# Performance work log

Hardware: AMD Instinct MI355X
Metric: run time of the kernel (lower is better)

## Reference

```python
import jax, jax.numpy as jnp
import numpy as np

HID = 256   # hidden_dim
P = 16      # pool_size
EPS = 1e-5


def _ln(x, g, b):
    m = x.mean(-1, keepdims=True)
    v = x.var(-1, keepdims=True)
    return (x - m) * jax.lax.rsqrt(v + EPS) * g + b


def setup_inputs() -> dict:
    key = jax.random.key(0)
    ks = jax.random.split(key, 12)
    B, Cf, H, W = 8, 512, 64, 64
    Cg = Cf // 2
    Co = Cf // 2
    s = 0.02
    d = {}
    d['e_f'] = jax.random.normal(ks[0], (B, Cf, H, W), jnp.float32)
    d['e_g'] = jax.random.normal(ks[1], (B, Cg, H, W), jnp.float32)
    d['l_feat'] = jax.random.normal(ks[2], (B, 768, 20), jnp.float32)
    d['l_mask'] = jnp.ones((B, 20, 1), jnp.float32)
    d['ln_f_g'] = jnp.ones((Cf,), jnp.float32)
    d['ln_f_b'] = jnp.zeros((Cf,), jnp.float32)
    d['ln_g_g'] = jnp.ones((Cg,), jnp.float32)
    d['ln_g_b'] = jnp.zeros((Cg,), jnp.float32)
    d['wq'] = jax.random.normal(ks[3], (Cf, HID), jnp.float32) * s
    d['bq'] = jnp.zeros((HID,), jnp.float32)
    d['wk'] = jax.random.normal(ks[4], (Cg, HID), jnp.float32) * s
    d['bk'] = jnp.zeros((HID,), jnp.float32)
    d['wv'] = jax.random.normal(ks[5], (Cg, HID), jnp.float32) * s
    d['bv'] = jnp.zeros((HID,), jnp.float32)
    d['wo'] = jax.random.normal(ks[6], (HID, HID), jnp.float32) * s
    d['bo'] = jnp.zeros((HID,), jnp.float32)
    d['dw_k'] = jax.random.normal(ks[7], (HID, 1, 3, 3), jnp.float32) * s  # depthwise kernel (OIHW, I=1)
    d['efp_w'] = jax.random.normal(ks[8], (HID, Cf), jnp.float32) * s     # 1x1 conv v_channels->hidden
    d['efp_b'] = jnp.zeros((HID,), jnp.float32)
    d['outc_w'] = jax.random.normal(ks[9], (Co, HID), jnp.float32) * s    # 1x1 conv hidden->out
    d['outc_b'] = jnp.zeros((Co,), jnp.float32)
    d['bn_g'] = jnp.ones((Co,), jnp.float32)
    d['bn_b'] = jnp.zeros((Co,), jnp.float32)
    d['bn_m'] = jnp.zeros((Co,), jnp.float32)
    d['bn_v'] = jnp.ones((Co,), jnp.float32)
    return d


def reference(e_f, e_g, l_feat, l_mask, ln_f_g, ln_f_b, ln_g_g, ln_g_b,
              wq, bq, wk, bk, wv, bv, wo, bo, dw_k, efp_w, efp_b,
              outc_w, outc_b, bn_g, bn_b, bn_m, bn_v):
    B, Cf, H, W = e_f.shape
    # Q = w_qi(LN(e_f))                                  (B, HW, HID)
    q = _ln(e_f.transpose(0, 2, 3, 1), ln_f_g, ln_f_b).reshape(B, H * W, Cf) @ wq + bq
    # K/V projections from LN(e_g)
    g = _ln(e_g.transpose(0, 2, 3, 1), ln_g_g, ln_g_b).reshape(B, H * W, -1)
    k = (g @ wk + bk).reshape(B, H, W, HID)
    v = (g @ wv + bv).reshape(B, H, W, HID)
    # 16x16 max/avg pooling -> (B, Hp*Wp, HID)
    k = jnp.max(k.reshape(B, H // P, P, W // P, P, HID), axis=(2, 4)).reshape(B, -1, HID)
    v = jnp.mean(v.reshape(B, H // P, P, W // P, P, HID), axis=(2, 4)).reshape(B, -1, HID)
    # pooled attention
    attn = jax.nn.softmax(jnp.einsum('bqd,bkd->bqk', q, k) * (HID ** -0.5), axis=-1)
    a_i = jnp.einsum('bqk,bkd->bqd', attn, v)  # (B, HW, HID)
    # depthwise 3x3 conv on Q (NCHW)
    q_nchw = q.reshape(B, H, W, HID).transpose(0, 3, 1, 2)
    dw = jax.lax.conv_general_dilated(q_nchw, dw_k, (1, 1), [(1, 1), (1, 1)],
                                      feature_group_count=HID)
    combined = dw + a_i.reshape(B, H, W, HID).transpose(0, 3, 1, 2)
    comb = combined.transpose(0, 2, 3, 1).reshape(B, H * W, HID) @ wo + bo
    comb = comb.reshape(B, H, W, HID).transpose(0, 3, 1, 2)
    # 1x1 proj of e_f, elementwise gate
    efp = jnp.einsum('bchw,oc->bohw', e_f, efp_w) + efp_b[None, :, None, None]
    e_a = efp * comb
    # out: 1x1 conv + BN (inference) + ReLU (dropout inactive in eval)
    out = jnp.einsum('bchw,oc->bohw', e_a, outc_w) + outc_b[None, :, None, None]
    scale = (bn_g * jax.lax.rsqrt(bn_v + EPS))[None, :, None, None]
    out = (out - bn_m[None, :, None, None]) * scale + bn_b[None, :, None, None]
    return jax.nn.relu(out)
```

## Files before the change

### kernel.cpp

```cpp
#include <hip/hip_runtime.h>
#include <math.h>

#define EPS 1e-5f

typedef __attribute__((ext_vector_type(8))) short bf16x8;
typedef __attribute__((ext_vector_type(4))) float f32x4;

__device__ __forceinline__ unsigned short f2bf(float f) {
    unsigned int u = __float_as_uint(f);
    u += 0x7fff + ((u >> 16) & 1);
    return (unsigned short)(u >> 16);
}
__device__ __forceinline__ float bf2f(unsigned short h) {
    return __uint_as_float(((unsigned int)h) << 16);
}
__device__ __forceinline__ float lof(unsigned int u) {
    return __uint_as_float(u << 16);
}
__device__ __forceinline__ float hif(unsigned int u) {
    return __uint_as_float(u & 0xffff0000u);
}
__device__ __forceinline__ void async16(void* lds, const void* g) {
    __builtin_amdgcn_global_load_lds(
        (const __attribute__((address_space(1))) unsigned int*)g,
        (__attribute__((address_space(3))) unsigned int*)lds, 16, 0, 0);
}

__global__ __launch_bounds__(256) void prep_all(
    const float* __restrict__ lnfg, const float* __restrict__ lnfb,
    const float* __restrict__ wq, const float* __restrict__ bq,
    const float* __restrict__ efpw, const float* __restrict__ efpb,
    const float* __restrict__ lngg, const float* __restrict__ lngb,
    const float* __restrict__ wk, const float* __restrict__ bk,
    const float* __restrict__ wv, const float* __restrict__ bv,
    const float* __restrict__ wo, const float* __restrict__ outcw,
    const float* __restrict__ outcb, const float* __restrict__ bng,
    const float* __restrict__ bnb, const float* __restrict__ bnm,
    const float* __restrict__ bnv, const float* __restrict__ dwk,
    unsigned short* __restrict__ Wb1t, unsigned short* __restrict__ Wb2t,
    unsigned short* __restrict__ Wot, unsigned short* __restrict__ Woc,
    float* __restrict__ dwt,
    float* __restrict__ cs1, float* __restrict__ cst1,
    float* __restrict__ cs2, float* __restrict__ cst2,
    float* __restrict__ scv, float* __restrict__ shv)
{
    int idx = blockIdx.x * 256 + threadIdx.x;
    if (idx < 262144) {
        int n = idx >> 9, k = idx & 511;
        float v = (n < 256) ? lnfg[k] * wq[k * 256 + n]
                            : efpw[(size_t)(n - 256) * 512 + k];
        Wb1t[idx] = f2bf(v);
    } else if (idx < 327680) {
        int j = idx - 262144; int n = j >> 8, k = j & 255;
        Wb2t[j] = f2bf(lngg[k] * wk[k * 256 + n]);
    } else if (idx < 393216) {
        int j = idx - 327680; int n = j >> 8, k = j & 255;
        Wot[j] = f2bf(wo[k * 256 + n]);
    } else if (idx < 458752) {
        int j = idx - 393216;
        Woc[j] = f2bf(outcw[j]);
    } else if (idx < 461056) {
        int j = idx - 458752; int tap = j >> 8, ch = j & 255;
        dwt[j] = dwk[ch * 9 + tap];
    } else if (idx < 462336) {
        int j = idx - 461056;
        if (j < 256) {
            int n = j; float cs = 0.f, ct = 0.f;
            for (int k = 0; k < 512; k++) {
                float w = wq[k * 256 + n];
                cs += lnfg[k] * w; ct += lnfb[k] * w;
            }
            cs1[n] = cs; cst1[n] = ct + bq[n];
        } else if (j < 512) {
            cs1[j] = 0.f; cst1[j] = efpb[j - 256];
        } else if (j < 768) {
            int n = j - 512; float cs = 0.f, ct = 0.f;
            for (int k = 0; k < 256; k++) {
                float w = wk[k * 256 + n];
                cs += lngg[k] * w; ct += lngb[k] * w;
            }
            cs2[n] = cs; cst2[n] = ct + bk[n];
        } else if (j < 1024) {
            int n = j - 768; float cs = 0.f, ct = 0.f;
            for (int k = 0; k < 256; k++) {
                float w = wv[k * 256 + n];
                cs += lngg[k] * w; ct += lngb[k] * w;
            }
            cs2[256 + n] = cs; cst2[256 + n] = ct + bv[n];
        } else {
            int n = j - 1024;
            float s = bng[n] * rsqrtf(bnv[n] + EPS);
            scv[n] = s;
            shv[n] = (outcb[n] - bnm[n]) * s + bnb[n];
        }
    }
}

__global__ __launch_bounds__(256) void transpose_fg(
    const float* __restrict__ ef, const float* __restrict__ eg,
    unsigned short* __restrict__ ef_bf, unsigned short* __restrict__ eg_bf,
    float* __restrict__ pf, float* __restrict__ pfq,
    float* __restrict__ pg, float* __restrict__ pgq)
{
    __shared__ float tile[64][65];
    __shared__ float psum[4][64], pss[4][64];
    int id = blockIdx.x;
    const float* src; unsigned short* dst; float* ps; float* pq;
    int C, cblk, b, p0;
    if (id < 4096) {
        src = ef; dst = ef_bf; ps = pf; pq = pfq; C = 512;
        p0 = (id & 63) * 64; cblk = (id >> 6) & 7; b = id >> 9;
    } else {
        id -= 4096;
        src = eg; dst = eg_bf; ps = pg; pq = pgq; C = 256;
        p0 = (id & 63) * 64; cblk = (id >> 6) & 3; b = id >> 8;
    }
    int c0 = cblk * 64;
    const float* s = src + ((size_t)b * C + c0) * 4096 + p0;
    int t = threadIdx.x;

    int cr = t >> 4, p4 = (t & 15) * 4;
#pragma unroll
    for (int i = 0; i < 4; i++) {
        int c = i * 16 + cr;
        float4 v = *(const float4*)(s + (size_t)c * 4096 + p4);
        tile[c][p4 + 0] = v.x; tile[c][p4 + 1] = v.y;
        tile[c][p4 + 2] = v.z; tile[c][p4 + 3] = v.w;
    }
    __syncthreads();

    unsigned short* d = dst + ((size_t)(b * 4096 + p0)) * C + c0;
    int pr = t >> 3, c8 = (t & 7) * 8;
#pragma unroll
    for (int i = 0; i < 2; i++) {
        int p = i * 32 + pr;
        uint4 pk;
        pk.x = (unsigned)f2bf(tile[c8 + 0][p]) | ((unsigned)f2bf(tile[c8 + 1][p]) << 16);
        pk.y = (unsigned)f2bf(tile[c8 + 2][p]) | ((unsigned)f2bf(tile[c8 + 3][p]) << 16);
        pk.z = (unsigned)f2bf(tile[c8 + 4][p]) | ((unsigned)f2bf(tile[c8 + 5][p]) << 16);
        pk.w = (unsigned)f2bf(tile[c8 + 6][p]) | ((unsigned)f2bf(tile[c8 + 7][p]) << 16);
        *(uint4*)(d + (size_t)p * C + c8) = pk;
    }

    int lane = t & 63, grp = t >> 6;
    float sm = 0.f, sq = 0.f;
#pragma unroll
    for (int j = 0; j < 16; j++) {
        float v = tile[grp * 16 + j][lane];
        sm += v; sq += v * v;
    }
    psum[grp][lane] = sm; pss[grp][lane] = sq;
    __syncthreads();
    if (t < 64) {
        float fs = psum[0][t] + psum[1][t] + psum[2][t] + psum[3][t];
        float fq = pss[0][t] + pss[1][t] + pss[2][t] + pss[3][t];
        ps[cblk * 32768 + b * 4096 + p0 + t] = fs;
        pq[cblk * 32768 + b * 4096 + p0 + t] = fq;
    }
}

__global__ __launch_bounds__(256) void ln_finalize(
    const float* __restrict__ pf, const float* __restrict__ pfq,
    const float* __restrict__ pg, const float* __restrict__ pgq,
    float* __restrict__ mf, float* __restrict__ rf,
    float* __restrict__ mg, float* __restrict__ rg)
{
    int gp = blockIdx.x * 256 + threadIdx.x;
    float s = 0.f, q = 0.f;
#pragma unroll
    for (int i = 0; i < 8; i++) { s += pf[i * 32768 + gp]; q += pfq[i * 32768 + gp]; }
    float m = s * (1.f / 512.f);
    float v = q * (1.f / 512.f) - m * m;
    mf[gp] = m; rf[gp] = rsqrtf(v + EPS);
    s = 0.f; q = 0.f;
#pragma unroll
    for (int i = 0; i < 4; i++) { s += pg[i * 32768 + gp]; q += pgq[i * 32768 + gp]; }
    m = s * (1.f / 256.f);
    v = q * (1.f / 256.f) - m * m;
    mg[gp] = m; rg[gp] = rsqrtf(v + EPS);
}

template<int K>
__device__ __forceinline__ void mfma_core(
    const unsigned short* __restrict__ A, const unsigned short* __restrict__ Bt,
    int m0, int n0, unsigned short* As, unsigned short* Bs, f32x4 acc[4][4])
{
    const int tid = threadIdx.x;
    const int wave = tid >> 6, lane = tid & 63;
    const int wm = (wave & 1) * 64, wn = (wave >> 1) * 64;
#pragma unroll
    for (int i = 0; i < 4; i++)
#pragma unroll
        for (int j = 0; j < 4; j++) acc[i][j] = (f32x4){0.f, 0.f, 0.f, 0.f};

    const int srow = wave * 32 + (lane >> 3);
    const int sg = (lane & 7) ^ ((lane >> 3) & 7);
    const unsigned short* ga = A + (size_t)(m0 + srow) * K + sg * 8;
    const unsigned short* gb = Bt + (size_t)(n0 + srow) * K + sg * 8;

    for (int k0 = 0; k0 < K; k0 += 64) {
#pragma unroll
        for (int t = 0; t < 4; t++) {
            async16(As + (wave * 32 + t * 8) * 64, ga + (size_t)t * 8 * K + k0);
            async16(Bs + (wave * 32 + t * 8) * 64, gb + (size_t)t * 8 * K + k0);
        }
        __syncthreads();
#pragma unroll
        for (int ks = 0; ks < 2; ks++) {
            bf16x8 af[4], bfr[4];
            int kb = ks * 4 + (lane >> 4);
            int slot = (kb ^ (lane & 7)) * 8;
#pragma unroll
            for (int i = 0; i < 4; i++) {
                int m = wm + i * 16 + (lane & 15);
                af[i] = *(const bf16x8*)&As[m * 64 + slot];
                int n = wn + i * 16 + (lane & 15);
                bfr[i] = *(const bf16x8*)&Bs[n * 64 + slot];
            }
#pragma unroll
            for (int i = 0; i < 4; i++)
#pragma unroll
                for (int j = 0; j < 4; j++)
                    acc[i][j] = __builtin_amdgcn_mfma_f32_16x16x32_bf16(
                        af[i], bfr[j], acc[i][j], 0, 0, 0);
        }
        __syncthreads();
    }
}

__global__ __launch_bounds__(256) void gemm1_mfma(
    const unsigned short* __restrict__ ef_bf, const unsigned short* __restrict__ Wb1t,
    const float* __restrict__ cs1, const float* __restrict__ cst1,
    const float* __restrict__ mf, const float* __restrict__ rf,
    unsigned short* __restrict__ qbuf, unsigned short* __restrict__ efpbuf)
{
    __shared__ unsigned short As[8192], Bs[8192];
    f32x4 acc[4][4];
    int m0 = blockIdx.x * 128, n0 = blockIdx.y * 128;
    mfma_core<512>(ef_bf, Wb1t, m0, n0, As, Bs, acc);
    int lane = threadIdx.x & 63, wave = threadIdx.x >> 6;
    int wm = (wave & 1) * 64, wn = (wave >> 1) * 64;
    bool isq = (n0 < 256);
#pragma unroll
    for (int i = 0; i < 4; i++) {
#pragma unroll
        for (int r = 0; r < 4; r++) {
            int gm = m0 + wm + i * 16 + ((lane >> 4) * 4) + r;
            float mean = mf[gm], rs = rf[gm];
#pragma unroll
            for (int j = 0; j < 4; j++) {
                int n = n0 + wn + j * 16 + (lane & 15);
                float v = acc[i][j][r];
                if (isq) {
                    float o = rs * (v - mean * cs1[n]) + cst1[n];
                    qbuf[(size_t)gm * 256 + n] = f2bf(o);
                } else {
                    efpbuf[(size_t)gm * 256 + (n - 256)] = f2bf(v + cst1[n]);
                }
            }
        }
    }
}

__global__ __launch_bounds__(256) void gemm2k_mfma(
    const unsigned short* __restrict__ eg_bf, const unsigned short* __restrict__ Wb2t,
    const float* __restrict__ cs2, const float* __restrict__ cst2,
    const float* __restrict__ mg, const float* __restrict__ rg,
    unsigned short* __restrict__ kfull)
{
    __shared__ unsigned short As[8192], Bs[8192];
    f32x4 acc[4][4];
    int m0 = blockIdx.x * 128, n0 = blockIdx.y * 128;
    mfma_core<256>(eg_bf, Wb2t, m0, n0, As, Bs, acc);
    int lane = threadIdx.x & 63, wave = threadIdx.x >> 6;
    int wm = (wave & 1) * 64, wn = (wave >> 1) * 64;
#pragma unroll
    for (int i = 0; i < 4; i++) {
#pragma unroll
        for (int r = 0; r < 4; r++) {
            int gm = m0 + wm + i * 16 + ((lane >> 4) * 4) + r;
            float mean = mg[gm], rs = rg[gm];
#pragma unroll
            for (int j = 0; j < 4; j++) {
                int n = n0 + wn + j * 16 + (lane & 15);
                float o = rs * (acc[i][j][r] - mean * cs2[n]) + cst2[n];
                kfull[(size_t)gm * 256 + n] = f2bf(o);
            }
        }
    }
}

__global__ __launch_bounds__(256) void gemm34_mfma(
    const unsigned short* __restrict__ comb, const unsigned short* __restrict__ Wot,
    const float* __restrict__ bo, const unsigned short* __restrict__ efp,
    const unsigned short* __restrict__ Woc,
    const float* __restrict__ scv, const float* __restrict__ shv,
    float* __restrict__ outp)
{
    __shared__ unsigned short As[64 * 64];
    __shared__ unsigned short Bs[256 * 64];
    __shared__ unsigned short eat[64 * 256];
    const int tid = threadIdx.x;
    const int wave = tid >> 6, lane = tid & 63;
    const int m0 = blockIdx.x * 64;

    const int srow = lane >> 3;
    const int sg = (lane & 7) ^ (srow & 7);

    f32x4 acc[4][4];
#pragma unroll
    for (int i = 0; i < 4; i++)
#pragma unroll
        for (int j = 0; j < 4; j++) acc[i][j] = (f32x4){0.f, 0.f, 0.f, 0.f};

    const unsigned short* ga = comb + (size_t)(m0 + wave * 16 + srow) * 256 + sg * 8;
    const unsigned short* gb = Wot + (size_t)(wave * 64 + srow) * 256 + sg * 8;

    for (int k0 = 0; k0 < 256; k0 += 64) {
#pragma unroll
        for (int t = 0; t < 2; t++)
            async16(As + (wave * 16 + t * 8) * 64, ga + (size_t)t * 8 * 256 + k0);
#pragma unroll
        for (int t = 0; t < 8; t++)
            async16(Bs + (wave * 64 + t * 8) * 64, gb + (size_t)t * 8 * 256 + k0);
        __syncthreads();
#pragma unroll
        for (int ks = 0; ks < 2; ks++) {
            bf16x8 af[4], bfr[4];
            int kb = ks * 4 + (lane >> 4);
            int slot = (kb ^ (lane & 7)) * 8;
#pragma unroll
            for (int i = 0; i < 4; i++) {
                af[i]  = *(const bf16x8*)&As[(i * 16 + (lane & 15)) * 64 + slot];
                bfr[i] = *(const bf16x8*)&Bs[(wave * 64 + i * 16 + (lane & 15)) * 64 + slot];
            }
#pragma unroll
            for (int i = 0; i < 4; i++)
#pragma unroll
                for (int j = 0; j < 4; j++)
                    acc[i][j] = __builtin_amdgcn_mfma_f32_16x16x32_bf16(
                        af[i], bfr[j], acc[i][j], 0, 0, 0);
        }
        __syncthreads();
    }

    float bo4[4];
#pragma unroll
    for (int j = 0; j < 4; j++) bo4[j] = bo[wave * 64 + j * 16 + (lane & 15)];
#pragma unroll
    for (int i = 0; i < 4; i++) {
#pragma unroll
        for (int r = 0; r < 4; r++) {
            int pos = i * 16 + ((lane >> 4) * 4) + r;
#pragma unroll
            for (int j = 0; j < 4; j++) {
                int n = wave * 64 + j * 16 + (lane & 15);
                float o = (acc[i][j][r] + bo4[j])
                          * bf2f(efp[(size_t)(m0 + pos) * 256 + n]);
                int o8 = j * 2 + ((lane >> 3) & 1);
                int slot = o8 ^ (pos & 7);
                eat[pos * 256 + wave * 64 + slot * 8 + (lane & 7)] = f2bf(o);
            }
        }
    }

    f32x4 acc2[4][4];
#pragma unroll
    for (int i = 0; i < 4; i++)
#pragma unroll
        for (int j = 0; j < 4; j++) acc2[i][j] = (f32x4){0.f, 0.f, 0.f, 0.f};

    const unsigned short* gw = Woc + (size_t)(wave * 64 + srow) * 256 + sg * 8;
    for (int k0 = 0; k0 < 256; k0 += 64) {
#pragma unroll
        for (int t = 0; t < 8; t++)
            async16(Bs + (wave * 64 + t * 8) * 64, gw + (size_t)t * 8 * 256 + k0);
        __syncthreads();
        int kc = k0 >> 6;
#pragma unroll
        for (int ks = 0; ks < 2; ks++) {
            bf16x8 af2[4], bf2_[4];
            int kb = ks * 4 + (lane >> 4);
            int slot = (kb ^ (lane & 7)) * 8;
#pragma unroll
            for (int i = 0; i < 4; i++) {
                af2[i]  = *(const bf16x8*)&Bs[(wave * 64 + i * 16 + (lane & 15)) * 64 + slot];
                bf2_[i] = *(const bf16x8*)&eat[(i * 16 + (lane & 15)) * 256 + kc * 64 + slot];
            }
#pragma unroll
            for (int i = 0; i < 4; i++)
#pragma unroll
                for (int j = 0; j < 4; j++)
                    acc2[i][j] = __builtin_amdgcn_mfma_f32_16x16x32_bf16(
                        af2[i], bf2_[j], acc2[i][j], 0, 0, 0);
        }
        __syncthreads();
    }

#pragma unroll
    for (int i = 0; i < 4; i++) {
#pragma unroll
        for (int r = 0; r < 4; r++) {
            int co = wave * 64 + i * 16 + ((lane >> 4) * 4) + r;
            float s = scv[co], hh = shv[co];
#pragma unroll
            for (int j = 0; j < 4; j++) {
                int p = m0 + j * 16 + (lane & 15);
                float o = fmaxf(fmaf(acc2[i][j][r], s, hh), 0.f);
                outp[((size_t)(p >> 12)) * 1048576 + (size_t)co * 4096 + (p & 4095)] = o;
            }
        }
    }
}

__global__ __launch_bounds__(256) void pool_phase(
    const unsigned short* __restrict__ kfull, const float* __restrict__ eg,
    const float* __restrict__ rg, const float* __restrict__ mg,
    unsigned short* __restrict__ kpb, float* __restrict__ s1,
    float* __restrict__ s0)
{
    __shared__ float smem[4352];
    int id = blockIdx.x;
    int t = threadIdx.x;
    if (id < 128) {
        int b = id >> 4, cell = id & 15;
        int hp = cell >> 2, wp = cell & 3;
        int g8 = t & 31, rr = t >> 5;
        float kmx[8];
#pragma unroll
        for (int j = 0; j < 8; j++) kmx[j] = -3.402823466e38f;
#pragma unroll
        for (int rsub = 0; rsub < 2; rsub++) {
            int r = rr * 2 + rsub;
            int prow = (hp * 16 + r) * 64 + wp * 16;
            for (int cl = 0; cl < 16; cl++) {
                size_t basei = ((size_t)(b * 4096 + prow + cl)) * 256 + g8 * 8;
                uint4 kv = *(const uint4*)(kfull + basei);
                kmx[0] = fmaxf(kmx[0], lof(kv.x)); kmx[1] = fmaxf(kmx[1], hif(kv.x));
                kmx[2] = fmaxf(kmx[2], lof(kv.y)); kmx[3] = fmaxf(kmx[3], hif(kv.y));
                kmx[4] = fmaxf(kmx[4], lof(kv.z)); kmx[5] = fmaxf(kmx[5], hif(kv.z));
                kmx[6] = fmaxf(kmx[6], lof(kv.w)); kmx[7] = fmaxf(kmx[7], hif(kv.w));
            }
        }
#pragma unroll
        for (int j = 0; j < 8; j++) smem[rr * 256 + g8 * 8 + j] = kmx[j];
        __syncthreads();
        float m = smem[t];
#pragma unroll
        for (int r2 = 1; r2 < 8; r2++) m = fmaxf(m, smem[r2 * 256 + t]);
        kpb[(size_t)(b * 16 + cell) * 256 + t] = f2bf(m);
    } else {
        int id2 = id - 128;
        int b = id2 >> 6, hp = (id2 >> 4) & 3, cgrp = id2 & 15;
        int rr = t >> 4, cq = t & 15, cx = cq >> 2;
        int p = (hp * 16 + rr) * 64 + cq * 4;
        float4 w4 = *(const float4*)&rg[b * 4096 + p];
        float part[16];
        const float* egb = eg + ((size_t)b * 256 + cgrp * 16) * 4096 + p;
#pragma unroll
        for (int cc = 0; cc < 16; cc++) {
            float4 v4 = *(const float4*)(egb + (size_t)cc * 4096);
            part[cc] = w4.x * v4.x + w4.y * v4.y + w4.z * v4.z + w4.w * v4.w;
        }
#pragma unroll
        for (int cc = 0; cc < 16; cc++) smem[t * 16 + cc] = part[cc];
        if (cgrp == 0) {
            float4 m4 = *(const float4*)&mg[b * 4096 + p];
            smem[4096 + t] = w4.x * m4.x + w4.y * m4.y + w4.z * m4.z + w4.w * m4.w;
        }
        __syncthreads();
        if (t < 64) {
            int cx2 = t >> 4, cc = t & 15;
            float sacc = 0.f;
#pragma unroll
            for (int rr2 = 0; rr2 < 16; rr2++)
#pragma unroll
                for (int dq = 0; dq < 4; dq++)
                    sacc += smem[(rr2 * 16 + cx2 * 4 + dq) * 16 + cc];
            s1[((size_t)(b * 16 + hp * 4 + cx2)) * 256 + cgrp * 16 + cc] = sacc;
        }
        if (cgrp == 0 && t < 4) {
            float sacc = 0.f;
#pragma unroll
            for (int rr2 = 0; rr2 < 16; rr2++)
#pragma unroll
                for (int dq = 0; dq < 4; dq++)
                    sacc += smem[4096 + rr2 * 16 + t * 4 + dq];
            s0[b * 16 + hp * 4 + t] = sacc;
        }
    }
}

__global__ __launch_bounds__(256) void vpool_gemm(
    const float* __restrict__ s1, const float* __restrict__ s0,
    const float* __restrict__ lngg, const float* __restrict__ wv,
    const float* __restrict__ cs2, const float* __restrict__ cst2,
    float* __restrict__ vp)
{
    int cell = blockIdx.x;
    int n = threadIdx.x;
    const float* s1r = s1 + (size_t)cell * 256;
    float acc = 0.f;
    for (int c = 0; c < 256; c++)
        acc = fmaf(lngg[c] * s1r[c], wv[c * 256 + n], acc);
    vp[(size_t)cell * 256 + n] = acc * (1.f / 256.f)
        - (s0[cell] * (1.f / 256.f)) * cs2[256 + n] + cst2[256 + n];
}

__global__ __launch_bounds__(256) void combined_dw(
    const unsigned short* __restrict__ qbuf, const unsigned short* __restrict__ kpb,
    const float* __restrict__ vp, const float* __restrict__ dwt,
    unsigned short* __restrict__ combined)
{
    __shared__ float attns[256];
    int wave = threadIdx.x >> 6, lane = threadIdx.x & 63;
    int id = blockIdx.x;
    int b = id & 7, seg = id >> 3;
    int pidx0 = seg * 16;

    if (wave == 0) {
        int fr = lane & 15, quad = lane >> 4;
        const unsigned short* qrow = qbuf + (size_t)(b * 4096 + pidx0 + fr) * 256 + quad * 8;
        const unsigned short* krow = kpb + (size_t)(b * 16 + fr) * 256 + quad * 8;
        f32x4 sacc = {0.f, 0.f, 0.f, 0.f};
#pragma unroll
        for (int ks = 0; ks < 8; ks++) {
            bf16x8 af = *(const bf16x8*)(qrow + ks * 32);
            bf16x8 bf_ = *(const bf16x8*)(krow + ks * 32);
            sacc = __builtin_amdgcn_mfma_f32_16x16x32_bf16(af, bf_, sacc, 0, 0, 0);
        }
#pragma unroll
        for (int r = 0; r < 4; r++) {
            float s = sacc[r] * 0.0625f;
            float mx = s;
#pragma unroll
            for (int off = 8; off >= 1; off >>= 1) mx = fmaxf(mx, __shfl_xor(mx, off));
            float e = __expf(s - mx);
            float sum = e;
#pragma unroll
            for (int off = 8; off >= 1; off >>= 1) sum += __shfl_xor(sum, off);
            attns[(quad * 4 + r) * 16 + fr] = e / sum;
        }
    }
    __syncthreads();

    int pidx = pidx0 + wave * 4;
    int h = pidx >> 6, w0 = pidx & 63;
    int o4 = lane * 4;

    float4 kreg[9];
#pragma unroll
    for (int tap = 0; tap < 9; tap++)
        kreg[tap] = *(const float4*)&dwt[tap * 256 + o4];

    float4 acc[4];
#pragma unroll
    for (int i = 0; i < 4; i++) acc[i] = (float4){0.f, 0.f, 0.f, 0.f};

    const float* arow = attns + (wave * 4) * 16;
#pragma unroll
    for (int c = 0; c < 16; c++) {
        float4 v = *(const float4*)&vp[(size_t)(b * 16 + c) * 256 + o4];
#pragma unroll
        for (int i = 0; i < 4; i++) {
            float a = arow[i * 16 + c];
            acc[i].x = fmaf(a, v.x, acc[i].x); acc[i].y = fmaf(a, v.y, acc[i].y);
            acc[i].z = fmaf(a, v.z, acc[i].z); acc[i].w = fmaf(a, v.w, acc[i].w);
        }
    }
#pragma unroll
    for (int dy = 0; dy < 3; dy++) {
        int hh = h + dy - 1;
        if (hh < 0 || hh > 63) continue;
        const unsigned short* qr = qbuf + ((size_t)(b * 4096 + hh * 64)) * 256;
        float4 ft[6];
#pragma unroll
        for (int c = 0; c < 6; c++) {
            int xx = w0 - 1 + c;
            if (xx < 0 || xx > 63) {
                ft[c] = (float4){0.f, 0.f, 0.f, 0.f};
            } else {
                uint2 qa = *(const uint2*)(qr + (size_t)xx * 256 + o4);
                ft[c] = (float4){lof(qa.x), hif(qa.x), lof(qa.y), hif(qa.y)};
            }
        }
#pragma unroll
        for (int dx = 0; dx < 3; dx++) {
            float4 kk = kreg[dy * 3 + dx];
#pragma unroll
            for (int i = 0; i < 4; i++) {
                float4 qv = ft[i + dx];
                acc[i].x = fmaf(qv.x, kk.x, acc[i].x);
                acc[i].y = fmaf(qv.y, kk.y, acc[i].y);
                acc[i].z = fmaf(qv.z, kk.z, acc[i].z);
                acc[i].w = fmaf(qv.w, kk.w, acc[i].w);
            }
        }
    }
#pragma unroll
    for (int i = 0; i < 4; i++) {
        uint2 pk;
        pk.x = (unsigned)f2bf(acc[i].x) | ((unsigned)f2bf(acc[i].y) << 16);
        pk.y = (unsigned)f2bf(acc[i].z) | ((unsigned)f2bf(acc[i].w) << 16);
        *(uint2*)(combined + ((size_t)(b * 4096 + pidx + i)) * 256 + o4) = pk;
    }
}

extern "C" void kernel_launch(void* const* d_in, const int* in_sizes, int n_in,
                              void* d_out, int out_size, void* d_ws, size_t ws_size,
                              hipStream_t stream)
{
    const float* e_f   = (const float*)d_in[0];
    const float* e_g   = (const float*)d_in[1];
    const float* lnfg  = (const float*)d_in[4];
    const float* lnfb  = (const float*)d_in[5];
    const float* lngg  = (const float*)d_in[6];
    const float* lngb  = (const float*)d_in[7];
    const float* wq    = (const float*)d_in[8];
    const float* bq    = (const float*)d_in[9];
    const float* wk    = (const float*)d_in[10];
    const float* bk    = (const float*)d_in[11];
    const float* wv    = (const float*)d_in[12];
    const float* bv    = (const float*)d_in[13];
    const float* wo    = (const float*)d_in[14];
    const float* bo    = (const float*)d_in[15];
    const float* dwk   = (const float*)d_in[16];
    const float* efpw  = (const float*)d_in[17];
    const float* efpb  = (const float*)d_in[18];
    const float* outcw = (const float*)d_in[19];
    const float* outcb = (const float*)d_in[20];
    const float* bng   = (const float*)d_in[21];
    const float* bnb   = (const float*)d_in[22];
    const float* bnm   = (const float*)d_in[23];
    const float* bnv   = (const float*)d_in[24];
    float* outp = (float*)d_out;

    char* base = (char*)d_ws;
    auto alloc = [&](size_t bytes) -> char* {
        char* r = base; base += (bytes + 255) & ~(size_t)255; return r;
    };
    float* pf    = (float*)alloc(8 * 32768 * 4);
    float* pfq   = (float*)alloc(8 * 32768 * 4);
    float* pg    = (float*)alloc(4 * 32768 * 4);
    float* pgq   = (float*)alloc(4 * 32768 * 4);
    float* mf    = (float*)alloc(32768 * 4);
    float* rf    = (float*)alloc(32768 * 4);
    float* mg    = (float*)alloc(32768 * 4);
    float* rg    = (float*)alloc(32768 * 4);
    float* cs1   = (float*)alloc(512 * 4);
    float* cst1  = (float*)alloc(512 * 4);
    float* cs2   = (float*)alloc(512 * 4);
    float* cst2  = (float*)alloc(512 * 4);
    float* scv   = (float*)alloc(256 * 4);
    float* shv   = (float*)alloc(256 * 4);
    float* dwt   = (float*)alloc(9 * 256 * 4);
    unsigned short* Wb1t = (unsigned short*)alloc(262144 * 2);
    unsigned short* Wb2t = (unsigned short*)alloc(65536 * 2);
    unsigned short* Wot  = (unsigned short*)alloc(65536 * 2);
    unsigned short* Woc  = (unsigned short*)alloc(65536 * 2);
    unsigned short* ef_bf = (unsigned short*)alloc((size_t)32768 * 512 * 2);
    unsigned short* eg_bf = (unsigned short*)alloc((size_t)32768 * 256 * 2);
    unsigned short* qbuf  = (unsigned short*)alloc((size_t)32768 * 256 * 2);
    unsigned short* efpbuf = (unsigned short*)alloc((size_t)32768 * 256 * 2);
    unsigned short* kfull = (unsigned short*)alloc((size_t)32768 * 256 * 2);
    unsigned short* kpb  = (unsigned short*)alloc(128 * 256 * 2);
    float* vp    = (float*)alloc(128 * 256 * 4);
    float* s1    = (float*)alloc(128 * 256 * 4);
    float* s0    = (float*)alloc(128 * 4);

    prep_all<<<1806, 256, 0, stream>>>(
        lnfg, lnfb, wq, bq, efpw, efpb, lngg, lngb, wk, bk, wv, bv, wo,
        outcw, outcb, bng, bnb, bnm, bnv, dwk,
        Wb1t, Wb2t, Wot, Woc, dwt, cs1, cst1, cs2, cst2, scv, shv);
    transpose_fg<<<6144, 256, 0, stream>>>(e_f, e_g, ef_bf, eg_bf,
                                           pf, pfq, pg, pgq);
    ln_finalize<<<128, 256, 0, stream>>>(pf, pfq, pg, pgq, mf, rf, mg, rg);
    gemm1_mfma<<<dim3(256, 4), 256, 0, stream>>>(ef_bf, Wb1t, cs1, cst1, mf, rf,
                                                 qbuf, efpbuf);
    gemm2k_mfma<<<dim3(256, 2), 256, 0, stream>>>(eg_bf, Wb2t, cs2, cst2, mg, rg,
                                                  kfull);
    pool_phase<<<640, 256, 0, stream>>>(kfull, e_g, rg, mg, kpb, s1, s0);
    vpool_gemm<<<128, 256, 0, stream>>>(s1, s0, lngg, wv, cs2, cst2, vp);
    combined_dw<<<2048, 256, 0, stream>>>(qbuf, kpb, vp, dwt, kfull);
    gemm34_mfma<<<512, 256, 0, stream>>>(kfull, Wot, bo, efpbuf,
                                         Woc, scv, shv, outp);
}
```

Before: 323.5 us.

## Widen gemm1 tile to 128x256 and double transpose work per block

gemm1 now computes a 128x256 output tile per block, each wave holding 4x8 MFMA accumulators. This halves the number of passes over the A operand (ef_bf), and each block's tile lies entirely in either the Q or the efp half. The transpose kernel now has each block handle two 64-pixel tiles, issuing all global loads up front to hide latency and halving the block count. The trade-off is higher register and LDS use per block in gemm1, which may reduce occupancy, and an extra barrier in the transpose kernel.

```diff
diff --git a/kernel.cpp b/kernel.cpp
--- a/kernel.cpp
+++ b/kernel.cpp
@@ -107,55 +107,68 @@
     int id = blockIdx.x;
     const float* src; unsigned short* dst; float* ps; float* pq;
     int C, cblk, b, p0;
-    if (id < 4096) {
+    if (id < 2048) {
         src = ef; dst = ef_bf; ps = pf; pq = pfq; C = 512;
-        p0 = (id & 63) * 64; cblk = (id >> 6) & 7; b = id >> 9;
+        b = id >> 8; cblk = (id >> 5) & 7; p0 = (id & 31) * 128;
     } else {
-        id -= 4096;
+        id -= 2048;
         src = eg; dst = eg_bf; ps = pg; pq = pgq; C = 256;
-        p0 = (id & 63) * 64; cblk = (id >> 6) & 3; b = id >> 8;
+        b = id >> 7; cblk = (id >> 5) & 3; p0 = (id & 31) * 128;
     }
     int c0 = cblk * 64;
     const float* s = src + ((size_t)b * C + c0) * 4096 + p0;
     int t = threadIdx.x;
-
     int cr = t >> 4, p4 = (t & 15) * 4;
-#pragma unroll
-    for (int i = 0; i < 4; i++) {
-        int c = i * 16 + cr;
-        float4 v = *(const float4*)(s + (size_t)c * 4096 + p4);
-        tile[c][p4 + 0] = v.x; tile[c][p4 + 1] = v.y;
-        tile[c][p4 + 2] = v.z; tile[c][p4 + 3] = v.w;
-    }
-    __syncthreads();
-
-    unsigned short* d = dst + ((size_t)(b * 4096 + p0)) * C + c0;
+    int lane = t & 63, grp = t >> 6;
     int pr = t >> 3, c8 = (t & 7) * 8;
-#pragma unroll
-    for (int i = 0; i < 2; i++) {
-        int p = i * 32 + pr;
-        uint4 pk;
-        pk.x = (unsigned)f2bf(tile[c8 + 0][p]) | ((unsigned)f2bf(tile[c8 + 1][p]) << 16);
-        pk.y = (unsigned)f2bf(tile[c8 + 2][p]) | ((unsigned)f2bf(tile[c8 + 3][p]) << 16);
-        pk.z = (unsigned)f2bf(tile[c8 + 4][p]) | ((unsigned)f2bf(tile[c8 + 5][p]) << 16);
-        pk.w = (unsigned)f2bf(tile[c8 + 6][p]) | ((unsigned)f2bf(tile[c8 + 7][p]) << 16);
-        *(uint4*)(d + (size_t)p * C + c8) = pk;
-    }
-
-    int lane = t & 63, grp = t >> 6;
-    float sm = 0.f, sq = 0.f;
-#pragma unroll
-    for (int j = 0; j < 16; j++) {
-        float v = tile[grp * 16 + j][lane];
-        sm += v; sq += v * v;
-    }
-    psum[grp][lane] = sm; pss[grp][lane] = sq;
-    __syncthreads();
-    if (t < 64) {
-        float fs = psum[0][t] + psum[1][t] + psum[2][t] + psum[3][t];
-        float fq = pss[0][t] + pss[1][t] + pss[2][t] + pss[3][t];
-        ps[cblk * 32768 + b * 4096 + p0 + t] = fs;
-        pq[cblk * 32768 + b * 4096 + p0 + t] = fq;
+
+    float4 r1[4], r2[4];
+#pragma unroll
+    for (int i = 0; i < 4; i++)
+        r1[i] = *(const float4*)(s + (size_t)(i * 16 + cr) * 4096 + p4);
+#pragma unroll
+    for (int i = 0; i < 4; i++)
+        r2[i] = *(const float4*)(s + (size_t)(i * 16 + cr) * 4096 + 64 + p4);
+
+#pragma unroll
+    for (int half = 0; half < 2; half++) {
+#pragma unroll
+        for (int i = 0; i < 4; i++) {
+            float4 v = half ? r2[i] : r1[i];
+            int c = i * 16 + cr;
+            tile[c][p4 + 0] = v.x; tile[c][p4 + 1] = v.y;
+            tile[c][p4 + 2] = v.z; tile[c][p4 + 3] = v.w;
+        }
+        __syncthreads();
+
+        int pbase = p0 + half * 64;
+        unsigned short* d = dst + ((size_t)(b * 4096 + pbase)) * C + c0;
+#pragma unroll
+        for (int i = 0; i < 2; i++) {
+            int p = i * 32 + pr;
+            uint4 pk;
+            pk.x = (unsigned)f2bf(tile[c8 + 0][p]) | ((unsigned)f2bf(tile[c8 + 1][p]) << 16);
+            pk.y = (unsigned)f2bf(tile[c8 + 2][p]) | ((unsigned)f2bf(tile[c8 + 3][p]) << 16);
+            pk.z = (unsigned)f2bf(tile[c8 + 4][p]) | ((unsigned)f2bf(tile[c8 + 5][p]) << 16);
+            pk.w = (unsigned)f2bf(tile[c8 + 6][p]) | ((unsigned)f2bf(tile[c8 + 7][p]) << 16);
+            *(uint4*)(d + (size_t)p * C + c8) = pk;
+        }
+
+        float sm = 0.f, sq = 0.f;
+#pragma unroll
+        for (int j = 0; j < 16; j++) {
+            float v = tile[grp * 16 + j][lane];
+            sm += v; sq += v * v;
+        }
+        psum[grp][lane] = sm; pss[grp][lane] = sq;
+        __syncthreads();
+        if (t < 64) {
+            float fs = psum[0][t] + psum[1][t] + psum[2][t] + psum[3][t];
+            float fq = pss[0][t] + pss[1][t] + pss[2][t] + pss[3][t];
+            ps[cblk * 32768 + b * 4096 + pbase + t] = fs;
+            pq[cblk * 32768 + b * 4096 + pbase + t] = fq;
+        }
+        if (half == 0) __syncthreads();
     }
 }
 
@@ -228,19 +241,59 @@
     }
 }
 
-__global__ __launch_bounds__(256) void gemm1_mfma(
+__global__ __launch_bounds__(256, 2) void gemm1_mfma(
     const unsigned short* __restrict__ ef_bf, const unsigned short* __restrict__ Wb1t,
     const float* __restrict__ cs1, const float* __restrict__ cst1,
     const float* __restrict__ mf, const float* __restrict__ rf,
     unsigned short* __restrict__ qbuf, unsigned short* __restrict__ efpbuf)
 {
-    __shared__ unsigned short As[8192], Bs[8192];
-    f32x4 acc[4][4];
-    int m0 = blockIdx.x * 128, n0 = blockIdx.y * 128;
-    mfma_core<512>(ef_bf, Wb1t, m0, n0, As, Bs, acc);
-    int lane = threadIdx.x & 63, wave = threadIdx.x >> 6;
-    int wm = (wave & 1) * 64, wn = (wave >> 1) * 64;
-    bool isq = (n0 < 256);
+    __shared__ unsigned short As[128 * 64];
+    __shared__ unsigned short Bs[256 * 64];
+    f32x4 acc[4][8];
+    const int tid = threadIdx.x;
+    const int wave = tid >> 6, lane = tid & 63;
+    const int wm = (wave & 1) * 64, wn = (wave >> 1) * 128;
+    const int m0 = blockIdx.x * 128, n0 = blockIdx.y * 256;
+#pragma unroll
+    for (int i = 0; i < 4; i++)
+#pragma unroll
+        for (int j = 0; j < 8; j++) acc[i][j] = (f32x4){0.f, 0.f, 0.f, 0.f};
+
+    const int srow = lane >> 3;
+    const int sg = (lane & 7) ^ (srow & 7);
+    const unsigned short* ga = ef_bf + (size_t)(m0 + wave * 32 + srow) * 512 + sg * 8;
+    const unsigned short* gb = Wb1t + (size_t)(n0 + wave * 64 + srow) * 512 + sg * 8;
+
+    for (int k0 = 0; k0 < 512; k0 += 64) {
+#pragma unroll
+        for (int t = 0; t < 4; t++)
+            async16(As + (wave * 32 + t * 8) * 64, ga + (size_t)t * 8 * 512 + k0);
+#pragma unroll
+        for (int t = 0; t < 8; t++)
+            async16(Bs + (wave * 64 + t * 8) * 64, gb + (size_t)t * 8 * 512 + k0);
+        __syncthreads();
+#pragma unroll
+        for (int ks = 0; ks < 2; ks++) {
+            bf16x8 af[4], bfr[8];
+            int kb = ks * 4 + (lane >> 4);
+            int slot = (kb ^ (lane & 7)) * 8;
+#pragma unroll
+            for (int i = 0; i < 4; i++)
+                af[i] = *(const bf16x8*)&As[(wm + i * 16 + (lane & 15)) * 64 + slot];
+#pragma unroll
+            for (int j = 0; j < 8; j++)
+                bfr[j] = *(const bf16x8*)&Bs[(wn + j * 16 + (lane & 15)) * 64 + slot];
+#pragma unroll
+            for (int i = 0; i < 4; i++)
+#pragma unroll
+                for (int j = 0; j < 8; j++)
+                    acc[i][j] = __builtin_amdgcn_mfma_f32_16x16x32_bf16(
+                        af[i], bfr[j], acc[i][j], 0, 0, 0);
+        }
+        __syncthreads();
+    }
+
+    bool isq = (n0 == 0);
 #pragma unroll
     for (int i = 0; i < 4; i++) {
 #pragma unroll
@@ -248,14 +301,16 @@
             int gm = m0 + wm + i * 16 + ((lane >> 4) * 4) + r;
             float mean = mf[gm], rs = rf[gm];
 #pragma unroll
-            for (int j = 0; j < 4; j++) {
-                int n = n0 + wn + j * 16 + (lane & 15);
+            for (int j = 0; j < 8; j++) {
+                int nn = wn + j * 16 + (lane & 15);
                 float v = acc[i][j][r];
                 if (isq) {
+                    int n = nn;
                     float o = rs * (v - mean * cs1[n]) + cst1[n];
-                    qbuf[(size_t)gm * 256 + n] = f2bf(o);
+                    qbuf[(size_t)gm * 256 + nn] = f2bf(o);
                 } else {
-                    efpbuf[(size_t)gm * 256 + (n - 256)] = f2bf(v + cst1[n]);
+                    int n = nn + 256;
+                    efpbuf[(size_t)gm * 256 + nn] = f2bf(v + cst1[n]);
                 }
             }
         }
@@ -672,10 +727,10 @@
         lnfg, lnfb, wq, bq, efpw, efpb, lngg, lngb, wk, bk, wv, bv, wo,
         outcw, outcb, bng, bnb, bnm, bnv, dwk,
         Wb1t, Wb2t, Wot, Woc, dwt, cs1, cst1, cs2, cst2, scv, shv);
-    transpose_fg<<<6144, 256, 0, stream>>>(e_f, e_g, ef_bf, eg_bf,
+    transpose_fg<<<3072, 256, 0, stream>>>(e_f, e_g, ef_bf, eg_bf,
                                            pf, pfq, pg, pgq);
     ln_finalize<<<128, 256, 0, stream>>>(pf, pfq, pg, pgq, mf, rf, mg, rg);
-    gemm1_mfma<<<dim3(256, 4), 256, 0, stream>>>(ef_bf, Wb1t, cs1, cst1, mf, rf,
+    gemm1_mfma<<<dim3(256, 2), 256, 0, stream>>>(ef_bf, Wb1t, cs1, cst1, mf, rf,
                                                  qbuf, efpbuf);
     gemm2k_mfma<<<dim3(256, 2), 256, 0, stream>>>(eg_bf, Wb2t, cs2, cst2, mg, rg,
                                                   kfull);
```

After: 316.7 us. 1.02x faster.
